# Kernel tuning notes

Measured on AMD Instinct MI355X. Metric: run time of the kernel, lower is better.

## Reference

```python
import jax, jax.numpy as jnp
import numpy as np

BLOCK = 128          # fp8 quantization block size (from linear_deepseek_v3)
FP8_MAX = 448.0      # max representable value of float8_e4m3fn
F8 = jnp.float8_e4m3fn
G, T, K, N = 8, 1024, 7168, 2048


def setup_inputs() -> dict:
    key = jax.random.key(0)
    kx, kw, kb = jax.random.split(key, 3)
    xs = jax.random.normal(kx, (G, T, K), jnp.float32)
    # Build an fp8 block-quantized weight + per-(128x128)-block fp32 scale,
    # matching the stored self.weight (fp8) and self.scale parameters.
    w_raw = jax.random.normal(kw, (G, N, K), jnp.float32)
    wb = w_raw.reshape(G, N // BLOCK, BLOCK, K // BLOCK, BLOCK)
    amax = jnp.max(jnp.abs(wb), axis=(2, 4))            # [G, NB, KB]
    scale = amax / FP8_MAX
    w_q = (wb / scale[:, :, None, :, None]).astype(F8).astype(jnp.float32)
    weight = w_q.reshape(G, N, K)                        # fp8 code values held in fp32
    bias = jax.random.normal(kb, (G, N), jnp.float32) * 0.02
    return {"xs": xs, "weight": weight, "scale": scale, "bias": bias}


def reference(xs, weight, scale, bias):
    """Grouped fp8 block-quantized GEMM with inline dequant.
    xs:     [G, T, K] fp32 activations (one slab per group)
    weight: [G, N, K] fp8-quantized weights (stored as fp32 code values)
    scale:  [G, N/128, K/128] fp32 per-block weight scales
    bias:   [G, N] fp32
    """
    g, t, k = xs.shape
    n = weight.shape[1]
    kb, nb = k // BLOCK, n // BLOCK
    # --- act_quant_deepseek_v3: per (token, 128-col block) absmax/448 scale ---
    xb = xs.reshape(g, t, kb, BLOCK)
    a_scale = jnp.max(jnp.abs(xb), axis=-1) / FP8_MAX        # [G, T, KB]
    x_q = (xb / a_scale[..., None]).astype(F8).astype(jnp.float32)
    x_deq = (x_q * a_scale[..., None]).reshape(g, t, k)      # fused dequant
    # --- weight dequant: broadcast per-(128x128)-block scale ---
    w_deq = (weight.reshape(g, nb, BLOCK, kb, BLOCK)
             * scale[:, :, None, :, None]).reshape(g, n, k)
    # --- grouped GEMM (y = x A^T) + bias, fp32 accumulation ---
    y = jnp.einsum('gtk,gnk->gtn', x_deq, w_deq) + bias[:, None, :]
    return y
```

## Files before the change

### kernel.cpp

```cpp
#include <hip/hip_runtime.h>
#include <hip/hip_bf16.h>
#include <stdint.h>

#define G_ 8
#define T_ 1024
#define K_ 7168
#define N_ 2048
#define KB_ (K_/128)
#define NB_ (N_/128)
#define NT8_ 56

typedef __attribute__((ext_vector_type(4))) float f32x4;
typedef __attribute__((ext_vector_type(8))) int   i32x8;

typedef __attribute__((address_space(3))) uint32_t lds_u32_t;
typedef const __attribute__((address_space(1))) uint32_t gbl_u32_t;

__device__ __forceinline__ void gload_lds16(const void* gsrc, const void* ldst)
{
    __builtin_amdgcn_global_load_lds(
        (gbl_u32_t*)(uintptr_t)gsrc,
        (lds_u32_t*)(uint32_t)(uintptr_t)ldst, 16, 0, 0);
}

__device__ __forceinline__ void blockbar()
{
    asm volatile("" ::: "memory");
    __builtin_amdgcn_s_barrier();
    asm volatile("" ::: "memory");
}

__global__ __launch_bounds__(256) void act_quant_kernel(
    const float* __restrict__ xs, uint8_t* __restrict__ xq8,
    float* __restrict__ ascale)
{
    const int grp = (blockIdx.x * 256 + threadIdx.x) >> 5;
    const int l   = threadIdx.x & 31;
    const size_t base = (size_t)grp * 128 + (size_t)l * 4;

    const float4 v = *(const float4*)(xs + base);
    float am = fmaxf(fmaxf(fabsf(v.x), fabsf(v.y)), fmaxf(fabsf(v.z), fabsf(v.w)));
#pragma unroll
    for (int off = 1; off <= 16; off <<= 1)
        am = fmaxf(am, __shfl_xor(am, off, 64));
    const float s = am / 448.0f;

    int pk = __builtin_amdgcn_cvt_pk_fp8_f32(v.x / s, v.y / s, 0, false);
    pk     = __builtin_amdgcn_cvt_pk_fp8_f32(v.z / s, v.w / s, pk, true);
    *(uint32_t*)(xq8 + base) = (uint32_t)pk;

    if (l == 0) {
        const int kb = grp % KB_;
        const int t  = (grp / KB_) & (T_ - 1);
        const int g  = grp / (KB_ * T_);
        ascale[(((size_t)(g * 4 + (t >> 8))) * KB_ + kb) * 256 + (t & 255)] = s;
    }
}

__global__ __launch_bounds__(256) void wrecode_kernel(
    const float* __restrict__ w, uint8_t* __restrict__ wq8)
{
    const size_t i = ((size_t)blockIdx.x * 256 + threadIdx.x) * 16;
    uint32_t o[4];
#pragma unroll
    for (int q = 0; q < 4; ++q) {
        const float4 a = *(const float4*)(w + i + q * 4);
        int pk = __builtin_amdgcn_cvt_pk_fp8_f32(a.x, a.y, 0, false);
        pk     = __builtin_amdgcn_cvt_pk_fp8_f32(a.z, a.w, pk, true);
        o[q] = (uint32_t)pk;
    }
    *(uint4*)(wq8 + i) = make_uint4(o[0], o[1], o[2], o[3]);
}

union Frag { i32x8 v; struct { int4 lo, hi; } p; };

#define RD_A(mh)                                                              \
  { _Pragma("unroll") for (int m = 0; m < 4; ++m) {                           \
      const int r  = wrow + ((mh)*4 + m)*16 + l15;                            \
      const int rx = (r & 7) << 4;                                            \
      const char* bp = smem + cb*32768 + r*128;                               \
      aF[m].p.lo = *(const int4*)(bp + ((lhi*32) ^ rx));                      \
      aF[m].p.hi = *(const int4*)(bp + ((lhi*32 + 16) ^ rx));                 \
      const float4 sv = *(const float4*)(smem + 131072 + ((u>>3)&1)*8192 +    \
          (u & 7)*1024 + (wrow + ((mh)*4 + m)*16 + lhi*4)*4);                 \
      asw[m][0] = sv.x*wsc; asw[m][1] = sv.y*wsc;                             \
      asw[m][2] = sv.z*wsc; asw[m][3] = sv.w*wsc;                             \
  } }

#define RD_B(nh)                                                              \
  { _Pragma("unroll") for (int n = 0; n < 2; ++n) {                           \
      const int r  = wcol + ((nh)*2 + n)*16 + l15;                            \
      const int rx = (r & 7) << 4;                                            \
      const char* bp = smem + 65536 + cb*32768 + r*128;                       \
      bF[(nh)*2+n].p.lo = *(const int4*)(bp + ((lhi*32) ^ rx));               \
      bF[(nh)*2+n].p.hi = *(const int4*)(bp + ((lhi*32 + 16) ^ rx));          \
  } }

#define MM(mh, nh)                                                            \
  { _Pragma("unroll") for (int m = 0; m < 4; ++m) {                           \
      _Pragma("unroll") for (int n = 0; n < 2; ++n) {                         \
        f32x4 blk = __builtin_amdgcn_mfma_scale_f32_16x16x128_f8f6f4(         \
            aF[m].v, bF[(nh)*2+n].v, z4, 0, 0,                                \
            0, 0x7F7F7F7F, 0, 0x7F7F7F7F);                                    \
        _Pragma("unroll") for (int j = 0; j < 4; ++j)                         \
          acc[(mh)*4+m][(nh)*2+n][j] += blk[j] * asw[m][j];                   \
  } } }

#define STG_A8(c, t, b) gload_lds16(pA8[c] + (size_t)(t)*128,                 \
      smem + (b)*32768 + (c)*8192 + tid*16)
#define STG_B8(c, t, b) gload_lds16(pB8[c] + (size_t)(t)*128,                 \
      smem + 65536 + (b)*32768 + (c)*8192 + tid*16)
#define STG_S(c) gload_lds16(pS + (size_t)(c)*2048,                           \
      smem + 131072 + ((c)&1)*8192 + tid*16)

__global__ __launch_bounds__(512) void gemm_fp8_kernel(
    const uint8_t* __restrict__ xq8, const uint8_t* __restrict__ wq8,
    const float* __restrict__ ascale, const float* __restrict__ wscale,
    const float* __restrict__ bias, float* __restrict__ y)
{
    __shared__ char smem[147456];

    const int bx0 = blockIdx.x;
    const int bx  = (bx0 & 7) * 32 + (bx0 >> 3);
    const int g   = bx >> 5;
    const int tm  = (bx >> 3) & 3;
    const int tn  = bx & 7;
    const int t0  = tm * 256, n0 = tn * 256;

    const int tid = threadIdx.x, lane = tid & 63, wid = tid >> 6;
    const int l15 = lane & 15, lhi = lane >> 4;
    const int wrow = (wid >> 2) * 128;
    const int wcol = (wid & 3) * 64;

    const uint8_t* Ag = xq8 + (size_t)g * T_ * K_;
    const uint8_t* Bg = wq8 + (size_t)g * N_ * K_;

    const int srow = tid >> 3;
    const int xoff = ((tid & 7) ^ (srow & 7)) * 16;
    const uint8_t* pA8[4];
    const uint8_t* pB8[4];
#pragma unroll
    for (int c = 0; c < 4; ++c) {
        pA8[c] = Ag + (size_t)(t0 + c * 64 + srow) * K_ + xoff;
        pB8[c] = Bg + (size_t)(n0 + c * 64 + srow) * K_ + xoff;
    }
    const float* pS = ascale + ((size_t)(g * 4 + tm) * KB_) * 256 + tid * 4;
    const int wscb = (g * NB_ + ((n0 + wcol) >> 7)) * KB_;

    const f32x4 z4 = {0.f, 0.f, 0.f, 0.f};
    f32x4 acc[8][4] = {};
    Frag aF[4], bF[4];
    float asw[4][4];

    STG_S(0);
#pragma unroll
    for (int c = 0; c < 4; ++c) { STG_A8(c, 0, 0); STG_B8(c, 0, 0); }
#pragma unroll
    for (int c = 0; c < 4; ++c) { STG_A8(c, 1, 1); STG_B8(c, 1, 1); }
    asm volatile("s_waitcnt vmcnt(8)" ::: "memory");
    blockbar();

    for (int u = 0; u < NT8_; ++u) {
        const int cb = u & 1;
        const bool pf = (u + 2 < NT8_);
        const float wsc = wscale[wscb + u];

        if ((u & 7) == 0 && u + 8 < NT8_) STG_S((u >> 3) + 1);
        RD_A(0); RD_B(0);
        blockbar();
        asm volatile("s_waitcnt lgkmcnt(0)" ::: "memory");
        __builtin_amdgcn_s_setprio(1);
        MM(0, 0);
        __builtin_amdgcn_s_setprio(0);
        blockbar();

        RD_B(1);
        if (pf) { STG_A8(0, u + 2, cb); STG_A8(2, u + 2, cb); }
        blockbar();
        asm volatile("s_waitcnt lgkmcnt(0)" ::: "memory");
        __builtin_amdgcn_s_setprio(1);
        MM(0, 1);
        __builtin_amdgcn_s_setprio(0);
        blockbar();

        RD_A(1);
        if (pf) { STG_B8(0, u + 2, cb); STG_B8(1, u + 2, cb); }
        blockbar();
        asm volatile("s_waitcnt lgkmcnt(0)" ::: "memory");
        __builtin_amdgcn_s_setprio(1);
        MM(1, 0);
        __builtin_amdgcn_s_setprio(0);
        blockbar();

        if (pf) { STG_A8(1, u + 2, cb); STG_A8(3, u + 2, cb);
                  STG_B8(2, u + 2, cb); STG_B8(3, u + 2, cb); }
        __builtin_amdgcn_s_setprio(1);
        MM(1, 1);
        __builtin_amdgcn_s_setprio(0);
        if (pf)                  asm volatile("s_waitcnt vmcnt(8)" ::: "memory");
        else if (u + 1 < NT8_)   asm volatile("s_waitcnt vmcnt(0)" ::: "memory");
        blockbar();
    }

    float* Yg = y + (size_t)g * T_ * N_;
#pragma unroll
    for (int n = 0; n < 4; ++n) {
        const int col = n0 + wcol + n * 16 + l15;
        const float bv = bias[g * N_ + col];
#pragma unroll
        for (int m = 0; m < 8; ++m) {
            const int r0 = t0 + wrow + m * 16 + lhi * 4;
#pragma unroll
            for (int j = 0; j < 4; ++j)
                Yg[(size_t)(r0 + j) * N_ + col] = acc[m][n][j] + bv;
        }
    }
}

extern "C" void kernel_launch(void* const* d_in, const int* in_sizes, int n_in,
                              void* d_out, int out_size, void* d_ws, size_t ws_size,
                              hipStream_t stream)
{
    const float* xs     = (const float*)d_in[0];
    const float* weight = (const float*)d_in[1];
    const float* scale  = (const float*)d_in[2];
    const float* bias   = (const float*)d_in[3];
    float* y = (float*)d_out;

    uint8_t* xq8   = (uint8_t*)d_ws;
    float*   ascl  = (float*)((char*)d_ws + 58720256);
    uint8_t* wq8   = (uint8_t*)((char*)d_ws + 60555264);

    act_quant_kernel<<<(G_ * T_ * KB_) / 8, 256, 0, stream>>>(xs, xq8, ascl);

    wrecode_kernel<<<(int)(((size_t)G_ * N_ * K_ / 16) / 256), 256, 0, stream>>>(
        weight, wq8);

    gemm_fp8_kernel<<<256, 512, 0, stream>>>(xq8, wq8, ascl, scale, bias, y);
}
```

Baseline: 373.2 us.

## Fuse fp32-to-fp8 weight recode into GEMM B-tile staging

Removes the separate weight recode kernel. The GEMM now loads fp32 weight rows into registers, converts them to fp8 and writes them into the swizzled LDS buffer, interleaved with the existing double-buffered pipeline. This drops a full write and re-read of the fp8 weight copy in global memory, but it makes the GEMM read four times as many weight bytes, adds register pressure from eight f32x4 staging registers, and adds extra vmcnt waits. The activation quant also replaces per-element division with a reciprocal multiply.

```diff
diff --git a/kernel.cpp b/kernel.cpp
--- a/kernel.cpp
+++ b/kernel.cpp
@@ -43,10 +43,12 @@
 #pragma unroll
     for (int off = 1; off <= 16; off <<= 1)
         am = fmaxf(am, __shfl_xor(am, off, 64));
-    const float s = am / 448.0f;
-
-    int pk = __builtin_amdgcn_cvt_pk_fp8_f32(v.x / s, v.y / s, 0, false);
-    pk     = __builtin_amdgcn_cvt_pk_fp8_f32(v.z / s, v.w / s, pk, true);
+
+    const float rs = 448.0f / am;
+    const float s  = am * (1.0f / 448.0f);
+
+    int pk = __builtin_amdgcn_cvt_pk_fp8_f32(v.x * rs, v.y * rs, 0, false);
+    pk     = __builtin_amdgcn_cvt_pk_fp8_f32(v.z * rs, v.w * rs, pk, true);
     *(uint32_t*)(xq8 + base) = (uint32_t)pk;
 
     if (l == 0) {
@@ -55,21 +57,6 @@
         const int g  = grp / (KB_ * T_);
         ascale[(((size_t)(g * 4 + (t >> 8))) * KB_ + kb) * 256 + (t & 255)] = s;
     }
-}
-
-__global__ __launch_bounds__(256) void wrecode_kernel(
-    const float* __restrict__ w, uint8_t* __restrict__ wq8)
-{
-    const size_t i = ((size_t)blockIdx.x * 256 + threadIdx.x) * 16;
-    uint32_t o[4];
-#pragma unroll
-    for (int q = 0; q < 4; ++q) {
-        const float4 a = *(const float4*)(w + i + q * 4);
-        int pk = __builtin_amdgcn_cvt_pk_fp8_f32(a.x, a.y, 0, false);
-        pk     = __builtin_amdgcn_cvt_pk_fp8_f32(a.z, a.w, pk, true);
-        o[q] = (uint32_t)pk;
-    }
-    *(uint4*)(wq8 + i) = make_uint4(o[0], o[1], o[2], o[3]);
 }
 
 union Frag { i32x8 v; struct { int4 lo, hi; } p; };
@@ -108,13 +95,33 @@
 
 #define STG_A8(c, t, b) gload_lds16(pA8[c] + (size_t)(t)*128,                 \
       smem + (b)*32768 + (c)*8192 + tid*16)
-#define STG_B8(c, t, b) gload_lds16(pB8[c] + (size_t)(t)*128,                 \
-      smem + 65536 + (b)*32768 + (c)*8192 + tid*16)
 #define STG_S(c) gload_lds16(pS + (size_t)(c)*2048,                           \
       smem + 131072 + ((c)&1)*8192 + tid*16)
 
+#define LOAD_B8(t, h)                                                         \
+  { _Pragma("unroll") for (int j = 0; j < 2; ++j) {                           \
+      const float* s_ = pWf[(h)*2+j] + (size_t)(t)*128;                       \
+      _Pragma("unroll") for (int q = 0; q < 4; ++q)                           \
+        br[j*4+q] = *(const f32x4*)(s_ + q*4);                                \
+  } }
+
+#define CVT_WRITE_B(h, b)                                                     \
+  { _Pragma("unroll") for (int j = 0; j < 2; ++j) {                           \
+      const int row_ = ((h)*2+j)*64 + brow;                                   \
+      uint32_t o_[4];                                                         \
+      _Pragma("unroll") for (int q = 0; q < 4; ++q) {                         \
+        int pk_ = __builtin_amdgcn_cvt_pk_fp8_f32(                            \
+            br[j*4+q][0], br[j*4+q][1], 0, false);                            \
+        pk_ = __builtin_amdgcn_cvt_pk_fp8_f32(                                \
+            br[j*4+q][2], br[j*4+q][3], pk_, true);                           \
+        o_[q] = (uint32_t)pk_;                                                \
+      }                                                                       \
+      *(uint4*)(smem + 65536 + (b)*32768 + row_*128 + bwslot) =               \
+          make_uint4(o_[0], o_[1], o_[2], o_[3]);                             \
+  } }
+
 __global__ __launch_bounds__(512) void gemm_fp8_kernel(
-    const uint8_t* __restrict__ xq8, const uint8_t* __restrict__ wq8,
+    const uint8_t* __restrict__ xq8, const float* __restrict__ w,
     const float* __restrict__ ascale, const float* __restrict__ wscale,
     const float* __restrict__ bias, float* __restrict__ y)
 {
@@ -133,17 +140,22 @@
     const int wcol = (wid & 3) * 64;
 
     const uint8_t* Ag = xq8 + (size_t)g * T_ * K_;
-    const uint8_t* Bg = wq8 + (size_t)g * N_ * K_;
+    const float*   Wg = w   + (size_t)g * N_ * K_;
 
     const int srow = tid >> 3;
     const int xoff = ((tid & 7) ^ (srow & 7)) * 16;
     const uint8_t* pA8[4];
-    const uint8_t* pB8[4];
-#pragma unroll
-    for (int c = 0; c < 4; ++c) {
+#pragma unroll
+    for (int c = 0; c < 4; ++c)
         pA8[c] = Ag + (size_t)(t0 + c * 64 + srow) * K_ + xoff;
-        pB8[c] = Bg + (size_t)(n0 + c * 64 + srow) * K_ + xoff;
-    }
+
+    const int brow   = tid >> 3;
+    const int bwslot = ((tid & 7) ^ (brow & 7)) * 16;
+    const float* pWf[4];
+#pragma unroll
+    for (int c = 0; c < 4; ++c)
+        pWf[c] = Wg + (size_t)(n0 + c * 64 + brow) * K_ + (tid & 7) * 16;
+
     const float* pS = ascale + ((size_t)(g * 4 + tm) * KB_) * 256 + tid * 4;
     const int wscb = (g * NB_ + ((n0 + wcol) >> 7)) * KB_;
 
@@ -151,13 +163,27 @@
     f32x4 acc[8][4] = {};
     Frag aF[4], bF[4];
     float asw[4][4];
-
+    f32x4 br[8];
+
+    LOAD_B8(0, 0);
+    asm volatile("s_waitcnt vmcnt(0)" ::: "memory");
+    CVT_WRITE_B(0, 0);
+    LOAD_B8(0, 1);
+    asm volatile("s_waitcnt vmcnt(0)" ::: "memory");
+    CVT_WRITE_B(1, 0);
+    LOAD_B8(1, 0);
+    asm volatile("s_waitcnt vmcnt(0)" ::: "memory");
+    CVT_WRITE_B(0, 1);
+    LOAD_B8(1, 1);
+    asm volatile("s_waitcnt vmcnt(0)" ::: "memory");
+    CVT_WRITE_B(1, 1);
     STG_S(0);
 #pragma unroll
-    for (int c = 0; c < 4; ++c) { STG_A8(c, 0, 0); STG_B8(c, 0, 0); }
-#pragma unroll
-    for (int c = 0; c < 4; ++c) { STG_A8(c, 1, 1); STG_B8(c, 1, 1); }
-    asm volatile("s_waitcnt vmcnt(8)" ::: "memory");
+    for (int c = 0; c < 4; ++c) STG_A8(c, 0, 0);
+#pragma unroll
+    for (int c = 0; c < 4; ++c) STG_A8(c, 1, 1);
+    asm volatile("s_waitcnt vmcnt(4)" ::: "memory");
+    asm volatile("s_waitcnt lgkmcnt(0)" ::: "memory");
     blockbar();
 
     for (int u = 0; u < NT8_; ++u) {
@@ -166,6 +192,7 @@
         const float wsc = wscale[wscb + u];
 
         if ((u & 7) == 0 && u + 8 < NT8_) STG_S((u >> 3) + 1);
+        if (pf) LOAD_B8(u + 2, 0);
         RD_A(0); RD_B(0);
         blockbar();
         asm volatile("s_waitcnt lgkmcnt(0)" ::: "memory");
@@ -174,8 +201,8 @@
         __builtin_amdgcn_s_setprio(0);
         blockbar();
 
+        if (pf) { STG_A8(0, u + 2, cb); STG_A8(2, u + 2, cb); }
         RD_B(1);
-        if (pf) { STG_A8(0, u + 2, cb); STG_A8(2, u + 2, cb); }
         blockbar();
         asm volatile("s_waitcnt lgkmcnt(0)" ::: "memory");
         __builtin_amdgcn_s_setprio(1);
@@ -184,7 +211,11 @@
         blockbar();
 
         RD_A(1);
-        if (pf) { STG_B8(0, u + 2, cb); STG_B8(1, u + 2, cb); }
+        if (pf) {
+            asm volatile("s_waitcnt vmcnt(2)" ::: "memory");
+            CVT_WRITE_B(0, cb);
+            LOAD_B8(u + 2, 1);
+        }
         blockbar();
         asm volatile("s_waitcnt lgkmcnt(0)" ::: "memory");
         __builtin_amdgcn_s_setprio(1);
@@ -192,13 +223,17 @@
         __builtin_amdgcn_s_setprio(0);
         blockbar();
 
-        if (pf) { STG_A8(1, u + 2, cb); STG_A8(3, u + 2, cb);
-                  STG_B8(2, u + 2, cb); STG_B8(3, u + 2, cb); }
+        if (pf) { STG_A8(1, u + 2, cb); STG_A8(3, u + 2, cb); }
         __builtin_amdgcn_s_setprio(1);
         MM(1, 1);
         __builtin_amdgcn_s_setprio(0);
-        if (pf)                  asm volatile("s_waitcnt vmcnt(8)" ::: "memory");
-        else if (u + 1 < NT8_)   asm volatile("s_waitcnt vmcnt(0)" ::: "memory");
+        if (pf) {
+            asm volatile("s_waitcnt vmcnt(2)" ::: "memory");
+            CVT_WRITE_B(1, cb);
+        } else if (u + 1 < NT8_) {
+            asm volatile("s_waitcnt vmcnt(0)" ::: "memory");
+        }
+        asm volatile("s_waitcnt lgkmcnt(0)" ::: "memory");
         blockbar();
     }
 
@@ -227,14 +262,9 @@
     const float* bias   = (const float*)d_in[3];
     float* y = (float*)d_out;
 
-    uint8_t* xq8   = (uint8_t*)d_ws;
-    float*   ascl  = (float*)((char*)d_ws + 58720256);
-    uint8_t* wq8   = (uint8_t*)((char*)d_ws + 60555264);
+    uint8_t* xq8  = (uint8_t*)d_ws;
+    float*   ascl = (float*)((char*)d_ws + 58720256);
 
     act_quant_kernel<<<(G_ * T_ * KB_) / 8, 256, 0, stream>>>(xs, xq8, ascl);
-
-    wrecode_kernel<<<(int)(((size_t)G_ * N_ * K_ / 16) / 256), 256, 0, stream>>>(
-        weight, wq8);
-
-    gemm_fp8_kernel<<<256, 512, 0, stream>>>(xq8, wq8, ascl, scale, bias, y);
-}
+    gemm_fp8_kernel<<<256, 512, 0, stream>>>(xq8, weight, ascl, scale, bias, y);
+}
```

Result: slower. 607.6 us (+62.8%).
